# Kernel optimization log

Hardware: AMD Instinct MI355X
Metric: run time of the kernel (lower is better)

The kernel has to match this reference:

```python
import jax, jax.numpy as jnp
import numpy as np

N_NODES = 50000
N_EDGES = 800000
N_GRAPHS = 512
IN_DIM = 128
HIDDEN = 64
N_CLASSES = 2


def gcn_conv(x, W, b, src, dst, n_nodes):
    """PyG GCNConv: add self-loops, symmetric deg^-1/2 normalization,
    linear transform then scatter-add aggregation at the target nodes."""
    xw = x @ W  # [N, out]
    loop = jnp.arange(n_nodes)
    s = jnp.concatenate([src, loop])  # sources incl. self-loops
    d = jnp.concatenate([dst, loop])  # targets incl. self-loops
    deg = jax.ops.segment_sum(jnp.ones(s.shape, xw.dtype), d, num_segments=n_nodes)
    dinv = jax.lax.rsqrt(jnp.where(deg > 0, deg, 1.0))
    norm = dinv[s] * dinv[d]  # [E+N]
    out = jax.ops.segment_sum(xw[s] * norm[:, None], d, num_segments=n_nodes)
    return out + b


def setup_inputs() -> dict:
    key = jax.random.key(0)
    ks = jax.random.split(key, 9)
    x = jax.random.normal(ks[0], (N_NODES, IN_DIM), dtype=jnp.float32)
    edge_index = jax.random.randint(ks[1], (2, N_EDGES), 0, N_NODES)
    batch = jnp.sort(jax.random.randint(ks[2], (N_NODES,), 0, N_GRAPHS))
    def glorot(k, fi, fo):
        return jax.random.normal(k, (fi, fo), dtype=jnp.float32) * (1.0 / np.sqrt(fi))
    W1 = glorot(ks[3], IN_DIM, HIDDEN)
    W2 = glorot(ks[4], HIDDEN, HIDDEN)
    W3 = glorot(ks[5], HIDDEN, N_CLASSES)
    b1 = jnp.zeros((HIDDEN,), jnp.float32)
    b2 = jnp.zeros((HIDDEN,), jnp.float32)
    b3 = jnp.zeros((N_CLASSES,), jnp.float32)
    return {"x": x, "edge_index": edge_index, "batch": batch,
            "W1": W1, "b1": b1, "W2": W2, "b2": b2, "W3": W3, "b3": b3}


def reference(x, edge_index, batch, W1, b1, W2, b2, W3, b3):
    # Eval mode: F.dropout(training=False) is identity.
    src, dst = edge_index[0], edge_index[1]
    z = jax.nn.relu(gcn_conv(x, W1, b1, src, dst, N_NODES))
    z = jax.nn.relu(gcn_conv(z, W2, b2, src, dst, N_NODES))
    z = gcn_conv(z, W3, b3, src, dst, N_NODES)  # [N, 2]
    # global_mean_pool over graph ids (only the last pooling result is returned)
    s = jax.ops.segment_sum(z, batch, num_segments=N_GRAPHS)
    cnt = jax.ops.segment_sum(jnp.ones((N_NODES,), z.dtype), batch, num_segments=N_GRAPHS)
    return s / jnp.clip(cnt, 1.0)[:, None]
```

## Files before the change

kernel.cpp:

```cpp
#include <hip/hip_runtime.h>
#include <hip/hip_bf16.h>

#define N_NODES   50000
#define N_EDGES   800000
#define N_GRAPHS  512
#define IN_DIM    128
#define HIDDEN    64
#define NPAD      50176
#define NBLK      196

__global__ __launch_bounds__(256) void k_degi(const int* __restrict__ dst,
                                              int* __restrict__ degi) {
    int e = blockIdx.x * 256 + threadIdx.x;
    if (e < N_EDGES) atomicAdd(&degi[dst[e]], 1);
}

__global__ __launch_bounds__(256) void k_dinv(const int* __restrict__ degi,
                                              float* __restrict__ dinv) {
    int i = blockIdx.x * 256 + threadIdx.x;
    if (i < N_NODES) dinv[i] = rsqrtf((float)degi[i] + 1.0f);
}

__global__ __launch_bounds__(256) void k_scan_block(const int* __restrict__ degi,
                                                    int* __restrict__ offs,
                                                    int* __restrict__ bsum) {
    __shared__ int sh[256];
    int tid = threadIdx.x;
    int i = blockIdx.x * 256 + tid;
    int v = degi[i];
    sh[tid] = v;
    __syncthreads();
    #pragma unroll
    for (int off = 1; off < 256; off <<= 1) {
        int t = (tid >= off) ? sh[tid - off] : 0;
        __syncthreads();
        sh[tid] += t;
        __syncthreads();
    }
    offs[i] = sh[tid] - v;
    if (tid == 255) bsum[blockIdx.x] = sh[tid];
}

__global__ __launch_bounds__(256) void k_scan_bsum(int* __restrict__ bsum,
                                                   int* __restrict__ boff) {
    __shared__ int sh[256];
    int tid = threadIdx.x;
    int v = (tid < NBLK) ? bsum[tid] : 0;
    sh[tid] = v;
    __syncthreads();
    #pragma unroll
    for (int off = 1; off < 256; off <<= 1) {
        int t = (tid >= off) ? sh[tid - off] : 0;
        __syncthreads();
        sh[tid] += t;
        __syncthreads();
    }
    if (tid < NBLK) boff[tid] = sh[tid] - v;
}

__global__ __launch_bounds__(256) void k_scan_add(int* __restrict__ offs,
                                                  const int* __restrict__ boff) {
    int i = blockIdx.x * 256 + threadIdx.x;
    offs[i] += boff[blockIdx.x];
}

__global__ __launch_bounds__(256) void k_fill(const int* __restrict__ src,
                                              const int* __restrict__ dst,
                                              const int* __restrict__ offs,
                                              int* __restrict__ cnt,
                                              int* __restrict__ csr_src) {
    int e = blockIdx.x * 256 + threadIdx.x;
    if (e >= N_EDGES) return;
    int d = dst[e];
    int pos = offs[d] + atomicAdd(&cnt[d], 1);
    csr_src[pos] = src[e];
}

template <int K, bool RELU_IN>
__global__ __launch_bounds__(256) void k_gemm64t(const float* __restrict__ A,
                                                 const float* __restrict__ W,
                                                 const float* __restrict__ bin,
                                                 const float* __restrict__ dinv,
                                                 float* __restrict__ out) {
    __shared__ float sA[64][65];
    __shared__ float sW[64][64];
    __shared__ float sB[64];

    const int tid = threadIdx.x;
    const int rowBase = blockIdx.x * 64;
    const int c0 = (tid & 15) * 4;
    const int r0 = (tid >> 4) * 4;

    if (RELU_IN && tid < 64) sB[tid] = bin[tid];

    float acc[4][4];
    #pragma unroll
    for (int j = 0; j < 4; ++j)
        #pragma unroll
        for (int c = 0; c < 4; ++c) acc[j][c] = 0.0f;

    for (int kc = 0; kc < K; kc += 64) {
        __syncthreads();
        #pragma unroll
        for (int p = 0; p < 4; ++p) {
            int i = p * 256 + tid;
            int k  = i >> 4;
            int cq = i & 15;
            *reinterpret_cast<float4*>(&sW[k][cq * 4]) =
                *reinterpret_cast<const float4*>(&W[(size_t)(kc + k) * 64 + cq * 4]);
        }
        #pragma unroll
        for (int p = 0; p < 4; ++p) {
            int i = p * 256 + tid;
            int row = i >> 4;
            int kq  = i & 15;
            int gr = rowBase + row;
            float4 v = make_float4(0.f, 0.f, 0.f, 0.f);
            if (gr < N_NODES)
                v = *reinterpret_cast<const float4*>(&A[(size_t)gr * K + kc + kq * 4]);
            if (RELU_IN) {
                v.x = fmaxf(v.x + sB[kq * 4 + 0], 0.f);
                v.y = fmaxf(v.y + sB[kq * 4 + 1], 0.f);
                v.z = fmaxf(v.z + sB[kq * 4 + 2], 0.f);
                v.w = fmaxf(v.w + sB[kq * 4 + 3], 0.f);
            }
            sA[row][kq * 4 + 0] = v.x;
            sA[row][kq * 4 + 1] = v.y;
            sA[row][kq * 4 + 2] = v.z;
            sA[row][kq * 4 + 3] = v.w;
        }
        __syncthreads();

        #pragma unroll 8
        for (int k = 0; k < 64; ++k) {
            float4 w4 = *reinterpret_cast<const float4*>(&sW[k][c0]);
            float a0 = sA[r0 + 0][k];
            float a1 = sA[r0 + 1][k];
            float a2 = sA[r0 + 2][k];
            float a3 = sA[r0 + 3][k];
            acc[0][0] = fmaf(a0, w4.x, acc[0][0]);
            acc[0][1] = fmaf(a0, w4.y, acc[0][1]);
            acc[0][2] = fmaf(a0, w4.z, acc[0][2]);
            acc[0][3] = fmaf(a0, w4.w, acc[0][3]);
            acc[1][0] = fmaf(a1, w4.x, acc[1][0]);
            acc[1][1] = fmaf(a1, w4.y, acc[1][1]);
            acc[1][2] = fmaf(a1, w4.z, acc[1][2]);
            acc[1][3] = fmaf(a1, w4.w, acc[1][3]);
            acc[2][0] = fmaf(a2, w4.x, acc[2][0]);
            acc[2][1] = fmaf(a2, w4.y, acc[2][1]);
            acc[2][2] = fmaf(a2, w4.z, acc[2][2]);
            acc[2][3] = fmaf(a2, w4.w, acc[2][3]);
            acc[3][0] = fmaf(a3, w4.x, acc[3][0]);
            acc[3][1] = fmaf(a3, w4.y, acc[3][1]);
            acc[3][2] = fmaf(a3, w4.z, acc[3][2]);
            acc[3][3] = fmaf(a3, w4.w, acc[3][3]);
        }
    }

    #pragma unroll
    for (int j = 0; j < 4; ++j) {
        int gr = rowBase + r0 + j;
        if (gr < N_NODES) {
            float di = dinv[gr];
            float4 o;
            o.x = di * acc[j][0];
            o.y = di * acc[j][1];
            o.z = di * acc[j][2];
            o.w = di * acc[j][3];
            *reinterpret_cast<float4*>(&out[(size_t)gr * 64 + c0]) = o;
        }
    }
}

__global__ __launch_bounds__(256) void k_gemm2(const float* __restrict__ A,
                                               const float* __restrict__ W3,
                                               const float* __restrict__ b2,
                                               const float* __restrict__ dinv,
                                               float* __restrict__ out) {
    __shared__ float sW[128];
    __shared__ float sB[64];
    int tid = threadIdx.x;
    if (tid < 128) sW[tid] = W3[tid];
    if (tid < 64)  sB[tid] = b2[tid];
    __syncthreads();
    int i = blockIdx.x * 256 + tid;
    if (i >= N_NODES) return;
    float a0 = 0.f, a1 = 0.f;
    const float* row = A + (size_t)i * 64;
    #pragma unroll
    for (int k = 0; k < 64; k += 4) {
        float4 v = *reinterpret_cast<const float4*>(row + k);
        float z;
        z = fmaxf(v.x + sB[k + 0], 0.f); a0 = fmaf(z, sW[(k+0)*2+0], a0); a1 = fmaf(z, sW[(k+0)*2+1], a1);
        z = fmaxf(v.y + sB[k + 1], 0.f); a0 = fmaf(z, sW[(k+1)*2+0], a0); a1 = fmaf(z, sW[(k+1)*2+1], a1);
        z = fmaxf(v.z + sB[k + 2], 0.f); a0 = fmaf(z, sW[(k+2)*2+0], a0); a1 = fmaf(z, sW[(k+2)*2+1], a1);
        z = fmaxf(v.w + sB[k + 3], 0.f); a0 = fmaf(z, sW[(k+3)*2+0], a0); a1 = fmaf(z, sW[(k+3)*2+1], a1);
    }
    float di = dinv[i];
    out[i * 2 + 0] = di * a0;
    out[i * 2 + 1] = di * a1;
}

__global__ __launch_bounds__(256) void k_gather64(const int* __restrict__ csr_src,
                                                  const int* __restrict__ offs,
                                                  const int* __restrict__ degi,
                                                  const float* __restrict__ dinv,
                                                  const float* __restrict__ yw,
                                                  float* __restrict__ agg) {
    int gid  = blockIdx.x * 256 + threadIdx.x;
    int node = gid >> 6;
    int lane = threadIdx.x & 63;
    if (node >= N_NODES) return;
    float acc = yw[(size_t)node * 64 + lane];
    int beg = offs[node];
    int n   = degi[node];
    int j = 0;
    for (; j + 7 < n; j += 8) {
        int s[8];
        #pragma unroll
        for (int u = 0; u < 8; ++u) s[u] = csr_src[beg + j + u];
        float v[8];
        #pragma unroll
        for (int u = 0; u < 8; ++u) v[u] = yw[(size_t)s[u] * 64 + lane];
        #pragma unroll
        for (int u = 0; u < 8; ++u) acc += v[u];
    }
    for (; j < n; ++j) {
        int s = csr_src[beg + j];
        acc += yw[(size_t)s * 64 + lane];
    }
    agg[(size_t)node * 64 + lane] = dinv[node] * acc;
}

__global__ __launch_bounds__(256) void k_gather2pool(const int* __restrict__ csr_src,
                                                     const int* __restrict__ offs,
                                                     const int* __restrict__ degi,
                                                     const float* __restrict__ dinv,
                                                     const float* __restrict__ yw,
                                                     const int* __restrict__ batch,
                                                     float* __restrict__ psum,
                                                     float* __restrict__ pcnt) {
    __shared__ float ls0[N_GRAPHS];
    __shared__ float ls1[N_GRAPHS];
    __shared__ float lc [N_GRAPHS];
    int tid = threadIdx.x;
    #pragma unroll
    for (int g = tid; g < N_GRAPHS; g += 256) {
        ls0[g] = 0.f; ls1[g] = 0.f; lc[g] = 0.f;
    }
    __syncthreads();

    int node = blockIdx.x * 256 + tid;
    if (node < N_NODES) {
        float2 v = *reinterpret_cast<const float2*>(&yw[(size_t)node * 2]);
        float a0 = v.x, a1 = v.y;
        int beg = offs[node];
        int n   = degi[node];
        for (int j = 0; j < n; ++j) {
            int s = csr_src[beg + j];
            float2 u = *reinterpret_cast<const float2*>(&yw[(size_t)s * 2]);
            a0 += u.x;
            a1 += u.y;
        }
        float di = dinv[node];
        int g = batch[node];
        atomicAdd(&ls0[g], di * a0);
        atomicAdd(&ls1[g], di * a1);
        atomicAdd(&lc [g], 1.0f);
    }
    __syncthreads();

    #pragma unroll
    for (int g = tid; g < N_GRAPHS; g += 256) {
        float c = lc[g];
        if (c != 0.0f) {
            atomicAdd(&psum[g * 2 + 0], ls0[g]);
            atomicAdd(&psum[g * 2 + 1], ls1[g]);
            atomicAdd(&pcnt[g], c);
        }
    }
}

__global__ __launch_bounds__(256) void k_final(const float* __restrict__ psum,
                                               const float* __restrict__ pcnt,
                                               const float* __restrict__ b3,
                                               float* __restrict__ out) {
    int g = blockIdx.x * 256 + threadIdx.x;
    if (g >= N_GRAPHS) return;
    float c  = pcnt[g];
    float cc = fmaxf(c, 1.0f);
    out[g * 2 + 0] = (psum[g * 2 + 0] + c * b3[0]) / cc;
    out[g * 2 + 1] = (psum[g * 2 + 1] + c * b3[1]) / cc;
}

extern "C" void kernel_launch(void* const* d_in, const int* in_sizes, int n_in,
                              void* d_out, int out_size, void* d_ws, size_t ws_size,
                              hipStream_t stream) {
    const float* x     = (const float*)d_in[0];
    const int*   ei    = (const int*)d_in[1];
    const int*   batch = (const int*)d_in[2];
    const float* W1    = (const float*)d_in[3];
    const float* b1    = (const float*)d_in[4];
    const float* W2    = (const float*)d_in[5];
    const float* b2    = (const float*)d_in[6];
    const float* W3    = (const float*)d_in[7];
    const float* b3    = (const float*)d_in[8];
    const int* src = ei;
    const int* dst = ei + N_EDGES;

    float* ws   = (float*)d_ws;
    float* dinv = ws;
    int*   degi = (int*)(dinv + NPAD);
    int*   offs = degi + NPAD;
    int*   cnt  = offs + NPAD;
    int*   bsum = cnt + NPAD;
    int*   boff = bsum + 256;
    int*   csr  = boff + 256;
    float* xw   = (float*)(csr + N_EDGES);
    float* agg  = xw + (size_t)N_NODES * 64;
    float* psum = agg + (size_t)N_NODES * 64;
    float* pcnt = psum + 1024;
    float* out  = (float*)d_out;

    hipMemsetAsync(degi, 0, NPAD * sizeof(int), stream);
    hipMemsetAsync(cnt,  0, NPAD * sizeof(int), stream);
    hipMemsetAsync(psum, 0, (1024 + 512) * sizeof(float), stream);

    k_degi<<<(N_EDGES + 255) / 256, 256, 0, stream>>>(dst, degi);
    k_dinv<<<(N_NODES + 255) / 256, 256, 0, stream>>>(degi, dinv);
    k_scan_block<<<NBLK, 256, 0, stream>>>(degi, offs, bsum);
    k_scan_bsum<<<1, 256, 0, stream>>>(bsum, boff);
    k_scan_add<<<NBLK, 256, 0, stream>>>(offs, boff);
    k_fill<<<(N_EDGES + 255) / 256, 256, 0, stream>>>(src, dst, offs, cnt, csr);

    k_gemm64t<128, false><<<(N_NODES + 63) / 64, 256, 0, stream>>>(x, W1, nullptr, dinv, xw);
    k_gather64<<<(N_NODES * 64) / 256, 256, 0, stream>>>(csr, offs, degi, dinv, xw, agg);

    k_gemm64t<64, true><<<(N_NODES + 63) / 64, 256, 0, stream>>>(agg, W2, b1, dinv, xw);
    k_gather64<<<(N_NODES * 64) / 256, 256, 0, stream>>>(csr, offs, degi, dinv, xw, agg);

    k_gemm2<<<(N_NODES + 255) / 256, 256, 0, stream>>>(agg, W3, b2, dinv, xw);
    k_gather2pool<<<(N_NODES + 255) / 256, 256, 0, stream>>>(csr, offs, degi, dinv, xw,
                                                             batch, psum, pcnt);

    k_final<<<(N_GRAPHS + 255) / 256, 256, 0, stream>>>(psum, pcnt, b3, out);
}
```

Baseline: 300.8 us.

## Shard degree and CSR-fill atomics by destination bucket across blocks

The degree count and CSR fill kernels now use 1024 blocks split into 8 shards. Each shard reads all edges but only applies atomics for destinations whose (d>>4)&7 matches its shard, meant to localize atomic traffic and reduce contention across caches or XCDs. The fill cursor is initialized with the scanned offsets inside k_scan_add, which removes a memset and the offs lookup in fill. In exchange, every edge is read eight times.

```diff
diff --git a/kernel.cpp b/kernel.cpp
--- a/kernel.cpp
+++ b/kernel.cpp
@@ -8,11 +8,17 @@
 #define HIDDEN    64
 #define NPAD      50176
 #define NBLK      196
-
-__global__ __launch_bounds__(256) void k_degi(const int* __restrict__ dst,
-                                              int* __restrict__ degi) {
-    int e = blockIdx.x * 256 + threadIdx.x;
-    if (e < N_EDGES) atomicAdd(&degi[dst[e]], 1);
+#define SHARD_BLOCKS 1024
+
+__global__ __launch_bounds__(256) void k_degi_sh(const int* __restrict__ dst,
+                                                 int* __restrict__ degi) {
+    const int shard = blockIdx.x & 7;
+    const int blk   = blockIdx.x >> 3;
+    const int nthr  = (SHARD_BLOCKS >> 3) * 256;
+    for (int e = blk * 256 + threadIdx.x; e < N_EDGES; e += nthr) {
+        int d = dst[e];
+        if (((d >> 4) & 7) == shard) atomicAdd(&degi[d], 1);
+    }
 }
 
 __global__ __launch_bounds__(256) void k_dinv(const int* __restrict__ degi,
@@ -59,21 +65,29 @@
 }
 
 __global__ __launch_bounds__(256) void k_scan_add(int* __restrict__ offs,
-                                                  const int* __restrict__ boff) {
+                                                  const int* __restrict__ boff,
+                                                  int* __restrict__ cnt) {
     int i = blockIdx.x * 256 + threadIdx.x;
-    offs[i] += boff[blockIdx.x];
-}
-
-__global__ __launch_bounds__(256) void k_fill(const int* __restrict__ src,
-                                              const int* __restrict__ dst,
-                                              const int* __restrict__ offs,
-                                              int* __restrict__ cnt,
-                                              int* __restrict__ csr_src) {
-    int e = blockIdx.x * 256 + threadIdx.x;
-    if (e >= N_EDGES) return;
-    int d = dst[e];
-    int pos = offs[d] + atomicAdd(&cnt[d], 1);
-    csr_src[pos] = src[e];
+    int v = offs[i] + boff[blockIdx.x];
+    offs[i] = v;
+    cnt[i]  = v;
+}
+
+__global__ __launch_bounds__(256) void k_fill_sh(const int* __restrict__ src,
+                                                 const int* __restrict__ dst,
+                                                 int* __restrict__ cnt,
+                                                 int* __restrict__ csr_src) {
+    const int shard = blockIdx.x & 7;
+    const int blk   = blockIdx.x >> 3;
+    const int nthr  = (SHARD_BLOCKS >> 3) * 256;
+    for (int e = blk * 256 + threadIdx.x; e < N_EDGES; e += nthr) {
+        int d = dst[e];
+        int s = src[e];
+        if (((d >> 4) & 7) == shard) {
+            int pos = atomicAdd(&cnt[d], 1);
+            csr_src[pos] = s;
+        }
+    }
 }
 
 template <int K, bool RELU_IN>
@@ -323,15 +337,14 @@
     float* out  = (float*)d_out;
 
     hipMemsetAsync(degi, 0, NPAD * sizeof(int), stream);
-    hipMemsetAsync(cnt,  0, NPAD * sizeof(int), stream);
     hipMemsetAsync(psum, 0, (1024 + 512) * sizeof(float), stream);
 
-    k_degi<<<(N_EDGES + 255) / 256, 256, 0, stream>>>(dst, degi);
+    k_degi_sh<<<SHARD_BLOCKS, 256, 0, stream>>>(dst, degi);
     k_dinv<<<(N_NODES + 255) / 256, 256, 0, stream>>>(degi, dinv);
     k_scan_block<<<NBLK, 256, 0, stream>>>(degi, offs, bsum);
     k_scan_bsum<<<1, 256, 0, stream>>>(bsum, boff);
-    k_scan_add<<<NBLK, 256, 0, stream>>>(offs, boff);
-    k_fill<<<(N_EDGES + 255) / 256, 256, 0, stream>>>(src, dst, offs, cnt, csr);
+    k_scan_add<<<NBLK, 256, 0, stream>>>(offs, boff, cnt);
+    k_fill_sh<<<SHARD_BLOCKS, 256, 0, stream>>>(src, dst, cnt, csr);
 
     k_gemm64t<128, false><<<(N_NODES + 63) / 64, 256, 0, stream>>>(x, W1, nullptr, dinv, xw);
     k_gather64<<<(N_NODES * 64) / 256, 256, 0, stream>>>(csr, offs, degi, dinv, xw, agg);
```

Result: faster. 294.5 us (-2.1%).
